# Optimization experiments

Measured on AMD Instinct MI355X. Metric: run time of the kernel, lower is better.

## Reference

```python
import jax, jax.numpy as jnp
import numpy as np

EMBED_DIM = 1024
NUM_HEADS = 16
HEAD_DIM = EMBED_DIM // NUM_HEADS
SCALING = HEAD_DIM ** -0.5


def setup_inputs() -> dict:
    key = jax.random.key(0)
    ks = jax.random.split(key, 10)
    B, S, D = 2, 2048, EMBED_DIM
    lim = 1.0 / np.sqrt(D)  # torch Linear default init scale
    def lin(k):
        kw, kb = jax.random.split(k)
        W = jax.random.uniform(kw, (D, D), jnp.float32, -lim, lim)
        b = jax.random.uniform(kb, (D,), jnp.float32, -lim, lim)
        return W, b
    Wq, bq = lin(ks[0])
    Wk, bk = lin(ks[1])
    Wv, bv = lin(ks[2])
    Wo, bo = lin(ks[3])
    hidden_states = jax.random.normal(ks[4], (B, S, D), jnp.float32)
    attention_mask = jnp.ones((B, S), jnp.int32)  # unused by the module's forward
    return {"hidden_states": hidden_states, "attention_mask": attention_mask,
            "Wq": Wq, "bq": bq, "Wk": Wk, "bk": bk, "Wv": Wv, "bv": bv,
            "Wo": Wo, "bo": bo}


def reference(hidden_states, attention_mask, Wq, bq, Wk, bk, Wv, bv, Wo, bo):
    B, S, D = hidden_states.shape
    H, hd = NUM_HEADS, HEAD_DIM

    def split_heads(x):  # [B,S,D] -> [B,H,S,hd]
        return x.reshape(B, S, H, hd).transpose(0, 2, 1, 3)

    q = split_heads(hidden_states @ Wq.T + bq) * SCALING
    k = split_heads(hidden_states @ Wk.T + bk)
    v = split_heads(hidden_states @ Wv.T + bv)

    scores = jnp.einsum("bhqd,bhkd->bhqk", q, k)  # [B,H,S,S]
    mask_value = jnp.finfo(scores.dtype).min
    causal = jnp.triu(jnp.ones((S, S), bool), k=1)  # True above diagonal
    scores = jnp.where(causal, mask_value, scores)
    probs = jax.nn.softmax(scores, axis=-1)

    out = jnp.einsum("bhqk,bhkd->bhqd", probs, v)  # [B,H,S,hd]
    out = out.transpose(0, 2, 1, 3).reshape(B, S, D)
    return out @ Wo.T + bo
```

## Files before the change

### kernel.cpp

```cpp
#include <hip/hip_runtime.h>


typedef __bf16 bf16;
typedef __attribute__((ext_vector_type(8))) __bf16 bf16x8;
typedef __attribute__((ext_vector_type(4))) __bf16 bf16x4;
typedef __attribute__((ext_vector_type(4))) float f32x4;

#define MFMA16(a, b, c) __builtin_amdgcn_mfma_f32_16x16x32_bf16((a), (b), (c), 0, 0, 0)

__device__ __forceinline__ void gl_lds16(const bf16* g, bf16* l) {
  __builtin_amdgcn_global_load_lds(
      (__attribute__((address_space(1))) void*)g,
      (__attribute__((address_space(3))) void*)l, 16, 0, 0);
}

__global__ __launch_bounds__(256) void cvt5(
    const float* __restrict__ x, const float* __restrict__ wq,
    const float* __restrict__ wk, const float* __restrict__ wv,
    const float* __restrict__ wo,
    bf16* __restrict__ xb, bf16* __restrict__ wqb, bf16* __restrict__ wkb,
    bf16* __restrict__ wvb, bf16* __restrict__ wob) {
  const int bx = blockIdx.x;
  const float* s;
  bf16* d;
  int base;
  if (bx < 4096)      { s = x;  d = xb;  base = bx; }
  else if (bx < 5120) { s = wq; d = wqb; base = bx - 4096; }
  else if (bx < 6144) { s = wk; d = wkb; base = bx - 5120; }
  else if (bx < 7168) { s = wv; d = wvb; base = bx - 6144; }
  else                { s = wo; d = wob; base = bx - 7168; }
  const int i = base * 1024 + threadIdx.x * 4;
  const float4 v = *(const float4*)(s + i);
  bf16x4 o;
  o[0] = (bf16)v.x; o[1] = (bf16)v.y; o[2] = (bf16)v.z; o[3] = (bf16)v.w;
  *(bf16x4*)(d + i) = o;
}

__global__ __launch_bounds__(256) void vtrans(const bf16* __restrict__ v,
                                              bf16* __restrict__ vt) {
  __shared__ bf16 Ts[64 * 80];
  const int t = threadIdx.x;
  const int st = blockIdx.x;
  const int bh = blockIdx.y;
  const int bb = bh >> 4, h = bh & 15;
  const bf16* src = v + ((size_t)bb * 2048 + st * 64) * 1024 + h * 64;
#pragma unroll
  for (int i = 0; i < 2; ++i) {
    const int idx = i * 256 + t;
    const int sl = idx >> 3, c = idx & 7;
    *(bf16x8*)&Ts[sl * 80 + c * 8] = *(const bf16x8*)(src + (size_t)sl * 1024 + c * 8);
  }
  __syncthreads();
  bf16* dst = vt + (size_t)bh * 64 * 2048 + st * 64;
#pragma unroll
  for (int i = 0; i < 2; ++i) {
    const int idx = i * 256 + t;
    const int d = idx >> 3, c2 = idx & 7;
    bf16x8 tmp;
#pragma unroll
    for (int e = 0; e < 8; ++e) tmp[e] = Ts[(c2 * 8 + e) * 80 + d];
    *(bf16x8*)(dst + (size_t)d * 2048 + c2 * 8) = tmp;
  }
}

template <int BM, typename OutT>
__global__ __launch_bounds__(256, 2) void gemm_bt3(
    const bf16* __restrict__ A,
    const bf16* __restrict__ W0, const bf16* __restrict__ W1, const bf16* __restrict__ W2,
    const float* __restrict__ B0, const float* __restrict__ B1, const float* __restrict__ B2,
    OutT* __restrict__ O0, OutT* __restrict__ O1, OutT* __restrict__ O2,
    float s0, float s1, float s2, int K) {
  constexpr int WM = BM / 32;
  __shared__ bf16 As[BM * 64];
  __shared__ bf16 Bs[128 * 64];

  const int t = threadIdx.x;
  const int lane = t & 63;
  const int wv = t >> 6;
  const int wm = wv & 1, wn = wv >> 1;
  const int qd = lane >> 4, ln = lane & 15;

  const int which = blockIdx.x >> 3;
  const bf16* W = (which == 0) ? W0 : (which == 1) ? W1 : W2;
  const float* Bi = (which == 0) ? B0 : (which == 1) ? B1 : B2;
  OutT* O = (which == 0) ? O0 : (which == 1) ? O1 : O2;
  const float scale = (which == 0) ? s0 : (which == 1) ? s1 : s2;

  const int n0 = (blockIdx.x & 7) * 128;
  const int m0 = blockIdx.y * BM;

  f32x4 acc[WM][4] = {};

  for (int k0 = 0; k0 < K; k0 += 64) {
#pragma unroll
    for (int i = 0; i < BM / 32; ++i) {
      const int s = i * 256 + t;
      const int row = s >> 3;
      const int c = (s & 7) ^ (row & 7);
      gl_lds16(A + (size_t)(m0 + row) * K + k0 + c * 8, &As[s * 8]);
    }
#pragma unroll
    for (int i = 0; i < 4; ++i) {
      const int s = i * 256 + t;
      const int row = s >> 3;
      const int c = (s & 7) ^ (row & 7);
      gl_lds16(W + (size_t)(n0 + row) * K + k0 + c * 8, &Bs[s * 8]);
    }
    __syncthreads();

#pragma unroll
    for (int ks = 0; ks < 2; ++ks) {
      bf16x8 af[WM], bw[4];
#pragma unroll
      for (int i = 0; i < WM; ++i) {
        const int r = wm * (BM / 2) + i * 16 + ln;
        af[i] = *(const bf16x8*)&As[r * 64 + (((ks * 4 + qd) ^ (ln & 7)) << 3)];
      }
#pragma unroll
      for (int j = 0; j < 4; ++j) {
        const int r = wn * 64 + j * 16 + ln;
        bw[j] = *(const bf16x8*)&Bs[r * 64 + (((ks * 4 + qd) ^ (ln & 7)) << 3)];
      }
#pragma unroll
      for (int i = 0; i < WM; ++i)
#pragma unroll
        for (int j = 0; j < 4; ++j)
          acc[i][j] = MFMA16(af[i], bw[j], acc[i][j]);
    }
    __syncthreads();
  }

#pragma unroll
  for (int i = 0; i < WM; ++i) {
    const int row = m0 + wm * (BM / 2) + i * 16 + qd * 4;
#pragma unroll
    for (int j = 0; j < 4; ++j) {
      const int col = n0 + wn * 64 + j * 16 + ln;
      const float bias = Bi[col];
#pragma unroll
      for (int r = 0; r < 4; ++r) {
        const float v = (acc[i][j][r] + bias) * scale;
        O[(size_t)(row + r) * 1024 + col] = (OutT)v;
      }
    }
  }
}

__global__ __launch_bounds__(256, 2) void attn_causal(
    const bf16* __restrict__ Q, const bf16* __restrict__ Kg,
    const bf16* __restrict__ VT, bf16* __restrict__ Ob) {
  __shared__ bf16 Ks[2][64 * 64];
  __shared__ bf16 Vts[2][64 * 64];
  __shared__ bf16 Ps[4][32 * 64];

  const int t = threadIdx.x;
  const int lane = t & 63;
  const int w = t >> 6;
  const int qd = lane >> 4, ln = lane & 15;

  const int blk = blockIdx.x;
  const int bh = blk & 31;
  const int g = blk >> 5;
  const int tq = (g < 8) ? (15 - g) : (g - 8);
  const int bb = bh >> 4, h = bh & 15;
  const size_t rowbase = (size_t)bb * 2048;
  const bf16* vtb = VT + (size_t)bh * 64 * 2048;

  const int q0 = tq * 128;
  const int nj = 2 * tq + 2;

  auto stage = [&](int buf, int j) {
    const bf16* kp = Kg + (rowbase + j * 64) * 1024 + h * 64;
#pragma unroll
    for (int i = 0; i < 2; ++i) {
      const int s = i * 256 + t;
      const int kv = s >> 3;
      const int c = (s & 7) ^ (kv & 7);
      gl_lds16(kp + (size_t)kv * 1024 + c * 8, &Ks[buf][s * 8]);
    }
#pragma unroll
    for (int i = 0; i < 2; ++i) {
      const int s = i * 256 + t;
      const int d = s >> 3;
      const int c = (s & 7) ^ (d & 7);
      gl_lds16(vtb + (size_t)d * 2048 + j * 64 + c * 8, &Vts[buf][s * 8]);
    }
  };

  const bf16* qp = Q + (rowbase + q0 + w * 32) * 1024 + h * 64;
  bf16x8 qf[2][2];
#pragma unroll
  for (int m = 0; m < 2; ++m)
#pragma unroll
    for (int ks = 0; ks < 2; ++ks)
      qf[m][ks] = *(const bf16x8*)(qp + (size_t)(m * 16 + ln) * 1024 + ks * 32 + qd * 8);

  float l_run[2][4] = {};
  f32x4 accO[2][4] = {};

  stage(0, 0);

#pragma unroll 1
  for (int j = 0; j < nj; ++j) {
    const int buf = j & 1;
    __syncthreads();
    if (j + 1 < nj) stage(buf ^ 1, j + 1);

    f32x4 accS[2][4] = {};
#pragma unroll
    for (int ks = 0; ks < 2; ++ks) {
#pragma unroll
      for (int nt = 0; nt < 4; ++nt) {
        const bf16x8 bk = *(const bf16x8*)
            &Ks[buf][(nt * 16 + ln) * 64 + (((ks * 4 + qd) ^ (ln & 7)) << 3)];
#pragma unroll
        for (int m = 0; m < 2; ++m)
          accS[m][nt] = MFMA16(qf[m][ks], bk, accS[m][nt]);
      }
    }

    if (j >= nj - 2) {
#pragma unroll
      for (int m = 0; m < 2; ++m)
#pragma unroll
        for (int r = 0; r < 4; ++r) {
          const int row = m * 16 + qd * 4 + r;
          const int qg = q0 + w * 32 + row;
          float sum = 0.f;
#pragma unroll
          for (int nt = 0; nt < 4; ++nt) {
            float p = __builtin_exp2f(accS[m][nt][r]);
            const int col = nt * 16 + ln;
            if ((j * 64 + col) > qg) p = 0.f;
            sum += p;
            Ps[w][row * 64 + ((((col >> 3) ^ (row & 7))) << 3) + (col & 7)] = (bf16)p;
          }
          l_run[m][r] += sum;
        }
    } else {
#pragma unroll
      for (int m = 0; m < 2; ++m)
#pragma unroll
        for (int r = 0; r < 4; ++r) {
          const int row = m * 16 + qd * 4 + r;
          float sum = 0.f;
#pragma unroll
          for (int nt = 0; nt < 4; ++nt) {
            const float p = __builtin_exp2f(accS[m][nt][r]);
            const int col = nt * 16 + ln;
            sum += p;
            Ps[w][row * 64 + ((((col >> 3) ^ (row & 7))) << 3) + (col & 7)] = (bf16)p;
          }
          l_run[m][r] += sum;
        }
    }

#pragma unroll
    for (int kt = 0; kt < 2; ++kt) {
      bf16x8 ap[2];
#pragma unroll
      for (int m = 0; m < 2; ++m)
        ap[m] = *(const bf16x8*)
            &Ps[w][(m * 16 + ln) * 64 + (((kt * 4 + qd) ^ (ln & 7)) << 3)];
#pragma unroll
      for (int nt = 0; nt < 4; ++nt) {
        const bf16x8 bv = *(const bf16x8*)
            &Vts[buf][(nt * 16 + ln) * 64 + (((kt * 4 + qd) ^ (ln & 7)) << 3)];
#pragma unroll
        for (int m = 0; m < 2; ++m)
          accO[m][nt] = MFMA16(ap[m], bv, accO[m][nt]);
      }
    }
  }

  bf16* op = Ob + (rowbase + q0 + w * 32) * 1024 + h * 64;
#pragma unroll
  for (int m = 0; m < 2; ++m) {
#pragma unroll
    for (int r = 0; r < 4; ++r) {
      float l = l_run[m][r];
#pragma unroll
      for (int off = 1; off < 16; off <<= 1) l += __shfl_xor(l, off, 64);
      const float inv_l = 1.0f / l;
#pragma unroll
      for (int nt = 0; nt < 4; ++nt)
        op[(size_t)(m * 16 + qd * 4 + r) * 1024 + nt * 16 + ln] =
            (bf16)(accO[m][nt][r] * inv_l);
    }
  }
}

extern "C" void kernel_launch(void* const* d_in, const int* in_sizes, int n_in,
                              void* d_out, int out_size, void* d_ws, size_t ws_size,
                              hipStream_t stream) {
  const float* X  = (const float*)d_in[0];
  const float* Wq = (const float*)d_in[2];
  const float* bq = (const float*)d_in[3];
  const float* Wk = (const float*)d_in[4];
  const float* bk = (const float*)d_in[5];
  const float* Wv = (const float*)d_in[6];
  const float* bv = (const float*)d_in[7];
  const float* Wo = (const float*)d_in[8];
  const float* bo = (const float*)d_in[9];
  float* out = (float*)d_out;

  bf16* xb  = (bf16*)d_ws;
  bf16* wqb = xb  + (size_t)4096 * 1024;
  bf16* wkb = wqb + (size_t)1024 * 1024;
  bf16* wvb = wkb + (size_t)1024 * 1024;
  bf16* wob = wvb + (size_t)1024 * 1024;
  bf16* q   = wob + (size_t)1024 * 1024;
  bf16* k   = q   + (size_t)4096 * 1024;
  bf16* v   = k   + (size_t)4096 * 1024;
  bf16* vt  = v   + (size_t)4096 * 1024;
  bf16* ao  = xb;

  const float scaling = 0.125f * 1.44269504088896f;

  dim3 blk(256);
  cvt5<<<dim3(8192), blk, 0, stream>>>(X, Wq, Wk, Wv, Wo, xb, wqb, wkb, wvb, wob);
  gemm_bt3<128, bf16><<<dim3(24, 32), blk, 0, stream>>>(
      xb, wqb, wkb, wvb, bq, bk, bv, q, k, v, scaling, 1.f, 1.f, 1024);
  vtrans<<<dim3(32, 32), blk, 0, stream>>>(v, vt);
  attn_causal<<<dim3(512), blk, 0, stream>>>(q, k, vt, ao);
  gemm_bt3<64, float><<<dim3(8, 64), blk, 0, stream>>>(
      ao, wob, wob, wob, bo, bo, bo, out, out, out, 1.f, 1.f, 1.f, 1024);
}
```

Before: 197.6 us.

## Split causal attention over KV chunks with atomic accumulation and fuse V transpose

Causal attention is split into KV chunks of 8 tiles, so long query tiles run on up to four blocks (1280 blocks instead of 512). Partial numerators and row sums are combined with float atomics, and a new normalize kernel divides and writes bf16. The separate V-transpose kernel is removed because the QKV GEMM epilogue now writes V already transposed. The change also uses raw v_exp_f32, sets s_setprio around the MFMA sections and raises occupancy to 3; this costs extra atomic traffic, a zero-init pass and one more launch.

```diff
diff --git a/kernel.cpp b/kernel.cpp
--- a/kernel.cpp
+++ b/kernel.cpp
@@ -12,6 +12,12 @@
   __builtin_amdgcn_global_load_lds(
       (__attribute__((address_space(1))) void*)g,
       (__attribute__((address_space(3))) void*)l, 16, 0, 0);
+}
+
+__device__ __forceinline__ float exp2_raw(float x) {
+  float r;
+  asm("v_exp_f32 %0, %1" : "=v"(r) : "v"(x));
+  return r;
 }
 
 __global__ __launch_bounds__(256) void cvt5(
@@ -19,8 +25,10 @@
     const float* __restrict__ wk, const float* __restrict__ wv,
     const float* __restrict__ wo,
     bf16* __restrict__ xb, bf16* __restrict__ wqb, bf16* __restrict__ wkb,
-    bf16* __restrict__ wvb, bf16* __restrict__ wob) {
+    bf16* __restrict__ wvb, bf16* __restrict__ wob,
+    float* __restrict__ oacc, float* __restrict__ lacc) {
   const int bx = blockIdx.x;
+  const int t = threadIdx.x;
   const float* s;
   bf16* d;
   int base;
@@ -29,38 +37,14 @@
   else if (bx < 6144) { s = wk; d = wkb; base = bx - 5120; }
   else if (bx < 7168) { s = wv; d = wvb; base = bx - 6144; }
   else                { s = wo; d = wob; base = bx - 7168; }
-  const int i = base * 1024 + threadIdx.x * 4;
+  const int i = base * 1024 + t * 4;
   const float4 v = *(const float4*)(s + i);
   bf16x4 o;
   o[0] = (bf16)v.x; o[1] = (bf16)v.y; o[2] = (bf16)v.z; o[3] = (bf16)v.w;
   *(bf16x4*)(d + i) = o;
-}
-
-__global__ __launch_bounds__(256) void vtrans(const bf16* __restrict__ v,
-                                              bf16* __restrict__ vt) {
-  __shared__ bf16 Ts[64 * 80];
-  const int t = threadIdx.x;
-  const int st = blockIdx.x;
-  const int bh = blockIdx.y;
-  const int bb = bh >> 4, h = bh & 15;
-  const bf16* src = v + ((size_t)bb * 2048 + st * 64) * 1024 + h * 64;
-#pragma unroll
-  for (int i = 0; i < 2; ++i) {
-    const int idx = i * 256 + t;
-    const int sl = idx >> 3, c = idx & 7;
-    *(bf16x8*)&Ts[sl * 80 + c * 8] = *(const bf16x8*)(src + (size_t)sl * 1024 + c * 8);
-  }
-  __syncthreads();
-  bf16* dst = vt + (size_t)bh * 64 * 2048 + st * 64;
-#pragma unroll
-  for (int i = 0; i < 2; ++i) {
-    const int idx = i * 256 + t;
-    const int d = idx >> 3, c2 = idx & 7;
-    bf16x8 tmp;
-#pragma unroll
-    for (int e = 0; e < 8; ++e) tmp[e] = Ts[(c2 * 8 + e) * 80 + d];
-    *(bf16x8*)(dst + (size_t)d * 2048 + c2 * 8) = tmp;
-  }
+  const float4 z = {0.f, 0.f, 0.f, 0.f};
+  if (t < 128)      ((float4*)oacc)[(size_t)bx * 128 + t] = z;
+  else if (t < 130) ((float4*)lacc)[bx * 2 + (t - 128)] = z;
 }
 
 template <int BM, typename OutT>
@@ -69,7 +53,7 @@
     const bf16* __restrict__ W0, const bf16* __restrict__ W1, const bf16* __restrict__ W2,
     const float* __restrict__ B0, const float* __restrict__ B1, const float* __restrict__ B2,
     OutT* __restrict__ O0, OutT* __restrict__ O1, OutT* __restrict__ O2,
-    float s0, float s1, float s2, int K) {
+    float s0, float s1, float s2, int K, int vt_which) {
   constexpr int WM = BM / 32;
   __shared__ bf16 As[BM * 64];
   __shared__ bf16 Bs[128 * 64];
@@ -137,18 +121,34 @@
     for (int j = 0; j < 4; ++j) {
       const int col = n0 + wn * 64 + j * 16 + ln;
       const float bias = Bi[col];
-#pragma unroll
-      for (int r = 0; r < 4; ++r) {
-        const float v = (acc[i][j][r] + bias) * scale;
-        O[(size_t)(row + r) * 1024 + col] = (OutT)v;
+      if (which == vt_which) {
+        const int bb = row >> 11, ss = row & 2047;
+        const int hh = col >> 6, dd = col & 63;
+        OutT* dst = O + ((size_t)((bb << 4) + hh) * 64 + dd) * 2048 + ss;
+        if constexpr (sizeof(OutT) == 2) {
+          bf16x4 pk;
+#pragma unroll
+          for (int r = 0; r < 4; ++r) pk[r] = (bf16)((acc[i][j][r] + bias) * scale);
+          *(bf16x4*)dst = pk;
+        } else {
+#pragma unroll
+          for (int r = 0; r < 4; ++r) dst[r] = (OutT)((acc[i][j][r] + bias) * scale);
+        }
+      } else {
+#pragma unroll
+        for (int r = 0; r < 4; ++r) {
+          const float v = (acc[i][j][r] + bias) * scale;
+          O[(size_t)(row + r) * 1024 + col] = (OutT)v;
+        }
       }
     }
   }
 }
 
-__global__ __launch_bounds__(256, 2) void attn_causal(
+__global__ __launch_bounds__(256, 3) void attn_causal(
     const bf16* __restrict__ Q, const bf16* __restrict__ Kg,
-    const bf16* __restrict__ VT, bf16* __restrict__ Ob) {
+    const bf16* __restrict__ VT, float* __restrict__ Oacc,
+    float* __restrict__ Lacc) {
   __shared__ bf16 Ks[2][64 * 64];
   __shared__ bf16 Vts[2][64 * 64];
   __shared__ bf16 Ps[4][32 * 64];
@@ -160,14 +160,21 @@
 
   const int blk = blockIdx.x;
   const int bh = blk & 31;
-  const int g = blk >> 5;
-  const int tq = (g < 8) ? (15 - g) : (g - 8);
+  const int g2 = blk >> 5;
+  int tq, ch;
+  if (g2 < 4)       { tq = g2;                 ch = 0; }
+  else if (g2 < 12) { tq = 4 + ((g2 - 4) >> 1); ch = (g2 - 4) & 1; }
+  else if (g2 < 24) { const int u = g2 - 12, qq = u / 3; tq = 8 + qq; ch = u - 3 * qq; }
+  else              { const int u = g2 - 24; tq = 12 + (u >> 2); ch = u & 3; }
+
   const int bb = bh >> 4, h = bh & 15;
   const size_t rowbase = (size_t)bb * 2048;
   const bf16* vtb = VT + (size_t)bh * 64 * 2048;
 
   const int q0 = tq * 128;
   const int nj = 2 * tq + 2;
+  const int j0 = ch * 8;
+  const int j1 = (j0 + 8 < nj) ? (j0 + 8) : nj;
 
   auto stage = [&](int buf, int j) {
     const bf16* kp = Kg + (rowbase + j * 64) * 1024 + h * 64;
@@ -198,15 +205,16 @@
   float l_run[2][4] = {};
   f32x4 accO[2][4] = {};
 
-  stage(0, 0);
+  stage(0, j0);
 
 #pragma unroll 1
-  for (int j = 0; j < nj; ++j) {
-    const int buf = j & 1;
+  for (int j = j0; j < j1; ++j) {
+    const int buf = (j - j0) & 1;
     __syncthreads();
-    if (j + 1 < nj) stage(buf ^ 1, j + 1);
+    if (j + 1 < j1) stage(buf ^ 1, j + 1);
 
     f32x4 accS[2][4] = {};
+    __builtin_amdgcn_s_setprio(1);
 #pragma unroll
     for (int ks = 0; ks < 2; ++ks) {
 #pragma unroll
@@ -218,6 +226,7 @@
           accS[m][nt] = MFMA16(qf[m][ks], bk, accS[m][nt]);
       }
     }
+    __builtin_amdgcn_s_setprio(0);
 
     if (j >= nj - 2) {
 #pragma unroll
@@ -229,7 +238,7 @@
           float sum = 0.f;
 #pragma unroll
           for (int nt = 0; nt < 4; ++nt) {
-            float p = __builtin_exp2f(accS[m][nt][r]);
+            float p = exp2_raw(accS[m][nt][r]);
             const int col = nt * 16 + ln;
             if ((j * 64 + col) > qg) p = 0.f;
             sum += p;
@@ -246,7 +255,7 @@
           float sum = 0.f;
 #pragma unroll
           for (int nt = 0; nt < 4; ++nt) {
-            const float p = __builtin_exp2f(accS[m][nt][r]);
+            const float p = exp2_raw(accS[m][nt][r]);
             const int col = nt * 16 + ln;
             sum += p;
             Ps[w][row * 64 + ((((col >> 3) ^ (row & 7))) << 3) + (col & 7)] = (bf16)p;
@@ -255,6 +264,7 @@
         }
     }
 
+    __builtin_amdgcn_s_setprio(1);
 #pragma unroll
     for (int kt = 0; kt < 2; ++kt) {
       bf16x8 ap[2];
@@ -271,9 +281,11 @@
           accO[m][nt] = MFMA16(ap[m], bv, accO[m][nt]);
       }
     }
+    __builtin_amdgcn_s_setprio(0);
   }
 
-  bf16* op = Ob + (rowbase + q0 + w * 32) * 1024 + h * 64;
+  float* oa = Oacc + ((size_t)bh * 2048 + q0 + w * 32) * 64;
+  float* la = Lacc + bh * 2048 + q0 + w * 32;
 #pragma unroll
   for (int m = 0; m < 2; ++m) {
 #pragma unroll
@@ -281,13 +293,29 @@
       float l = l_run[m][r];
 #pragma unroll
       for (int off = 1; off < 16; off <<= 1) l += __shfl_xor(l, off, 64);
-      const float inv_l = 1.0f / l;
+      const int row = m * 16 + qd * 4 + r;
+      if (ln == 0) atomicAdd(&la[row], l);
 #pragma unroll
       for (int nt = 0; nt < 4; ++nt)
-        op[(size_t)(m * 16 + qd * 4 + r) * 1024 + nt * 16 + ln] =
-            (bf16)(accO[m][nt][r] * inv_l);
+        atomicAdd(&oa[(size_t)row * 64 + nt * 16 + ln], accO[m][nt][r]);
     }
   }
+}
+
+__global__ __launch_bounds__(256) void onorm(const float* __restrict__ Oacc,
+                                             const float* __restrict__ Lacc,
+                                             bf16* __restrict__ ao) {
+  const int row = blockIdx.x;
+  const int t = threadIdx.x;
+  const int h = t >> 4, dq = t & 15;
+  const int bb = row >> 11, s = row & 2047;
+  const int bh = (bb << 4) + h;
+  const float inv = 1.0f / Lacc[bh * 2048 + s];
+  const float4 v = *(const float4*)&Oacc[((size_t)bh * 2048 + s) * 64 + dq * 4];
+  bf16x4 o;
+  o[0] = (bf16)(v.x * inv); o[1] = (bf16)(v.y * inv);
+  o[2] = (bf16)(v.z * inv); o[3] = (bf16)(v.w * inv);
+  *(bf16x4*)&ao[(size_t)row * 1024 + h * 64 + dq * 4] = o;
 }
 
 extern "C" void kernel_launch(void* const* d_in, const int* in_sizes, int n_in,
@@ -311,18 +339,20 @@
   bf16* wob = wvb + (size_t)1024 * 1024;
   bf16* q   = wob + (size_t)1024 * 1024;
   bf16* k   = q   + (size_t)4096 * 1024;
-  bf16* v   = k   + (size_t)4096 * 1024;
-  bf16* vt  = v   + (size_t)4096 * 1024;
+  bf16* vt  = k   + (size_t)4096 * 1024;
+  float* oacc = (float*)(vt + (size_t)4096 * 1024);
+  float* lacc = oacc + (size_t)4096 * 1024;
   bf16* ao  = xb;
 
   const float scaling = 0.125f * 1.44269504088896f;
 
   dim3 blk(256);
-  cvt5<<<dim3(8192), blk, 0, stream>>>(X, Wq, Wk, Wv, Wo, xb, wqb, wkb, wvb, wob);
+  cvt5<<<dim3(8192), blk, 0, stream>>>(X, Wq, Wk, Wv, Wo, xb, wqb, wkb, wvb, wob,
+                                       oacc, lacc);
   gemm_bt3<128, bf16><<<dim3(24, 32), blk, 0, stream>>>(
-      xb, wqb, wkb, wvb, bq, bk, bv, q, k, v, scaling, 1.f, 1.f, 1024);
-  vtrans<<<dim3(32, 32), blk, 0, stream>>>(v, vt);
-  attn_causal<<<dim3(512), blk, 0, stream>>>(q, k, vt, ao);
+      xb, wqb, wkb, wvb, bq, bk, bv, q, k, vt, scaling, 1.f, 1.f, 1024, 2);
+  attn_causal<<<dim3(1280), blk, 0, stream>>>(q, k, vt, oacc, lacc);
+  onorm<<<dim3(4096), blk, 0, stream>>>(oacc, lacc, ao);
   gemm_bt3<64, float><<<dim3(8, 64), blk, 0, stream>>>(
-      ao, wob, wob, wob, bo, bo, bo, out, out, out, 1.f, 1.f, 1.f, 1024);
-}
+      ao, wob, wob, wob, bo, bo, bo, out, out, out, 1.f, 1.f, 1.f, 1024, -1);
+}
```

New measurement: 194.5 us. No clear change (-1.5%).
